# Kernel optimization log

Measured on AMD Instinct MI355X. Metric: run time of the kernel, lower is better.

The kernel has to match this reference:

```python
import jax, jax.numpy as jnp
import numpy as np

N_EMBED = 1024
N_HEAD = 16
B, T = 4, 2048
EPS = 1e-5


def setup_inputs() -> dict:
    key = jax.random.key(0)
    ks = jax.random.split(key, 8)
    s = 0.02
    return {
        "x": jax.random.normal(ks[0], (B, T, N_EMBED), dtype=jnp.float32),
        "ln1_w": jnp.ones((N_EMBED,), jnp.float32),
        "ln1_b": jnp.zeros((N_EMBED,), jnp.float32),
        "w_qkv": jax.random.normal(ks[1], (N_EMBED, 3 * N_EMBED), dtype=jnp.float32) * s,
        "b_qkv": jnp.zeros((3 * N_EMBED,), jnp.float32),
        "w_o": jax.random.normal(ks[2], (N_EMBED, N_EMBED), dtype=jnp.float32) * s,
        "b_o": jnp.zeros((N_EMBED,), jnp.float32),
        "ln2_w": jnp.ones((N_EMBED,), jnp.float32),
        "ln2_b": jnp.zeros((N_EMBED,), jnp.float32),
        "w_fc": jax.random.normal(ks[3], (N_EMBED, 4 * N_EMBED), dtype=jnp.float32) * s,
        "b_fc": jnp.zeros((4 * N_EMBED,), jnp.float32),
        "w_proj": jax.random.normal(ks[4], (4 * N_EMBED, N_EMBED), dtype=jnp.float32) * s,
        "b_proj": jnp.zeros((N_EMBED,), jnp.float32),
    }


def _layernorm(x, w, b):
    mu = jnp.mean(x, axis=-1, keepdims=True)
    var = jnp.mean(jnp.square(x - mu), axis=-1, keepdims=True)
    return (x - mu) * jax.lax.rsqrt(var + EPS) * w + b


def _attention(x, w_qkv, b_qkv, w_o, b_o):
    b, t, c = x.shape
    hd = c // N_HEAD
    qkv = x @ w_qkv + b_qkv                      # [B,T,3C]
    q, k, v = jnp.split(qkv, 3, axis=-1)
    # [B,H,T,hd]
    q = q.reshape(b, t, N_HEAD, hd).transpose(0, 2, 1, 3)
    k = k.reshape(b, t, N_HEAD, hd).transpose(0, 2, 1, 3)
    v = v.reshape(b, t, N_HEAD, hd).transpose(0, 2, 1, 3)
    scale = 1.0 / np.sqrt(hd).astype(np.float32)
    scores = jnp.einsum('bhqd,bhkd->bhqk', q, k) * scale  # [B,H,T,T]
    mask = jnp.tril(jnp.ones((t, t), dtype=bool))
    scores = jnp.where(mask, scores, -jnp.inf)
    attn = jax.nn.softmax(scores, axis=-1)
    ctx = jnp.einsum('bhqk,bhkd->bhqd', attn, v)  # [B,H,T,hd]
    ctx = ctx.transpose(0, 2, 1, 3).reshape(b, t, c)
    return ctx @ w_o + b_o


def reference(x, ln1_w, ln1_b, w_qkv, b_qkv, w_o, b_o,
              ln2_w, ln2_b, w_fc, b_fc, w_proj, b_proj):
    # x = x + attn(ln1(x))
    x = x + _attention(_layernorm(x, ln1_w, ln1_b), w_qkv, b_qkv, w_o, b_o)
    # x = x + mlp(ln2(x))
    h = _layernorm(x, ln2_w, ln2_b)
    h = jax.nn.gelu(h @ w_fc + b_fc, approximate=False)
    x = x + (h @ w_proj + b_proj)
    return x
```

## Files before the change

kernel.cpp:

```cpp
#include <hip/hip_runtime.h>
#include <hip/hip_bf16.h>
#include <math.h>

#define N_EMBED 1024
#define N_HEAD 16
#define HD 64
#define BB 4
#define TT 2048
#define NTOK (BB * TT)
#define QKV_LD (3 * N_EMBED)

typedef __bf16 bf16x8 __attribute__((ext_vector_type(8)));
typedef float f32x4 __attribute__((ext_vector_type(4)));

__device__ __forceinline__ unsigned short f2bf(float f) {
    __hip_bfloat16 h = __float2bfloat16(f);
    return __builtin_bit_cast(unsigned short, h);
}

__device__ __forceinline__ void gll16(const unsigned short* g, unsigned short* l) {
    __builtin_amdgcn_global_load_lds(
        (const __attribute__((address_space(1))) void*)g,
        (__attribute__((address_space(3))) void*)l,
        16, 0, 0);
}

__global__ __launch_bounds__(256) void transpose_bf16_kernel(
    const float* __restrict__ in, unsigned short* __restrict__ out, int K, int N) {
    __shared__ float tile[32][33];
    int bx = blockIdx.x * 32;
    int by = blockIdx.y * 32;
    int tx = threadIdx.x, ty = threadIdx.y;
#pragma unroll
    for (int i = ty; i < 32; i += 8)
        tile[i][tx] = in[(size_t)(by + i) * N + bx + tx];
    __syncthreads();
#pragma unroll
    for (int i = ty; i < 32; i += 8)
        out[(size_t)(bx + i) * K + by + tx] = f2bf(tile[tx][i]);
}

__global__ __launch_bounds__(256) void transpose_v_kernel(
    const unsigned short* __restrict__ qkv, unsigned short* __restrict__ vt) {
    __shared__ unsigned short tile[32][33];
    int z = blockIdx.z;
    int b = z >> 4, h = z & 15;
    int t0 = blockIdx.x * 32, d0 = blockIdx.y * 32;
    int tx = threadIdx.x, ty = threadIdx.y;
    const unsigned short* src = qkv + (size_t)(b * TT) * QKV_LD + 2 * N_EMBED + h * HD;
#pragma unroll
    for (int i = ty; i < 32; i += 8)
        tile[i][tx] = src[(size_t)(t0 + i) * QKV_LD + d0 + tx];
    __syncthreads();
    unsigned short* dst = vt + (size_t)z * HD * TT;
#pragma unroll
    for (int i = ty; i < 32; i += 8)
        dst[(size_t)(d0 + i) * TT + t0 + tx] = tile[tx][i];
}

__global__ __launch_bounds__(256) void ln_kernel(
    const float* __restrict__ x, const float* __restrict__ w,
    const float* __restrict__ b, unsigned short* __restrict__ out) {
    int row = blockIdx.x;
    int t = threadIdx.x;
    const float* xr = x + (size_t)row * N_EMBED;
    float4 v = reinterpret_cast<const float4*>(xr)[t];
    float s = v.x + v.y + v.z + v.w;
    float s2 = v.x * v.x + v.y * v.y + v.z * v.z + v.w * v.w;
#pragma unroll
    for (int m = 1; m < 64; m <<= 1) {
        s += __shfl_xor(s, m);
        s2 += __shfl_xor(s2, m);
    }
    __shared__ float red[8];
    int wv = t >> 6, ln = t & 63;
    if (ln == 0) { red[wv] = s; red[wv + 4] = s2; }
    __syncthreads();
    s = red[0] + red[1] + red[2] + red[3];
    s2 = red[4] + red[5] + red[6] + red[7];
    float mu = s * (1.0f / N_EMBED);
    float var = s2 * (1.0f / N_EMBED) - mu * mu;
    float r = rsqrtf(var + 1e-5f);
    float4 wv4 = reinterpret_cast<const float4*>(w)[t];
    float4 bv4 = reinterpret_cast<const float4*>(b)[t];
    ushort4 o;
    o.x = f2bf((v.x - mu) * r * wv4.x + bv4.x);
    o.y = f2bf((v.y - mu) * r * wv4.y + bv4.y);
    o.z = f2bf((v.z - mu) * r * wv4.z + bv4.z);
    o.w = f2bf((v.w - mu) * r * wv4.w + bv4.w);
    *reinterpret_cast<ushort4*>(out + (size_t)row * N_EMBED + t * 4) = o;
}

template <int EPI>
__global__ __launch_bounds__(256) void gemm_kernel(
    const unsigned short* __restrict__ A,
    const unsigned short* __restrict__ BT,
    const float* __restrict__ bias,
    const float* __restrict__ resid,
    float* __restrict__ outf,
    unsigned short* __restrict__ outb,
    int M, int N, int K) {
    __shared__ __align__(16) unsigned short As[128 * 32];
    __shared__ __align__(16) unsigned short Bs[128 * 32];
    int nbn = N >> 7;
    int nwg = gridDim.x;
    int orig = blockIdx.x;
    int swz = (orig & 7) * (nwg >> 3) + (orig >> 3);
    int bm = swz / nbn, bn = swz % nbn;
    int t = threadIdx.x;
    int lane = t & 63, wv = t >> 6;
    int wm = wv >> 1, wn = wv & 1;
    int mr = lane & 15, kg = lane >> 4;

    f32x4 acc[4][4];
#pragma unroll
    for (int i = 0; i < 4; i++)
#pragma unroll
        for (int j = 0; j < 4; j++) acc[i][j] = (f32x4){0.f, 0.f, 0.f, 0.f};

    int srow = t >> 2, sq = t & 3;
    const unsigned short* gA1 = A + (size_t)(bm * 128 + srow) * K + sq * 8;
    const unsigned short* gA2 = gA1 + (size_t)64 * K;
    const unsigned short* gB1 = BT + (size_t)(bn * 128 + srow) * K + sq * 8;
    const unsigned short* gB2 = gB1 + (size_t)64 * K;
    int w512 = (t >> 6) * 512;

    for (int k0 = 0; k0 < K; k0 += 32) {
        __syncthreads();
        gll16(gA1 + k0, As + w512);
        gll16(gA2 + k0, As + 2048 + w512);
        gll16(gB1 + k0, Bs + w512);
        gll16(gB2 + k0, Bs + 2048 + w512);
        __syncthreads();
        bf16x8 af[4], bfr[4];
#pragma unroll
        for (int i = 0; i < 4; i++)
            af[i] = *reinterpret_cast<const bf16x8*>(&As[(wm * 64 + i * 16 + mr) * 32 + kg * 8]);
#pragma unroll
        for (int j = 0; j < 4; j++)
            bfr[j] = *reinterpret_cast<const bf16x8*>(&Bs[(wn * 64 + j * 16 + mr) * 32 + kg * 8]);
#pragma unroll
        for (int i = 0; i < 4; i++)
#pragma unroll
            for (int j = 0; j < 4; j++)
                acc[i][j] = __builtin_amdgcn_mfma_f32_16x16x32_bf16(af[i], bfr[j], acc[i][j], 0, 0, 0);
    }

#pragma unroll
    for (int i = 0; i < 4; i++)
#pragma unroll
        for (int j = 0; j < 4; j++) {
            int n = bn * 128 + wn * 64 + j * 16 + mr;
            float bs = bias[n];
#pragma unroll
            for (int r = 0; r < 4; r++) {
                int m = bm * 128 + wm * 64 + i * 16 + kg * 4 + r;
                size_t idx = (size_t)m * N + n;
                float v = acc[i][j][r] + bs;
                if (EPI == 0) {
                    outb[idx] = f2bf(v);
                } else if (EPI == 1) {
                    outf[idx] = v + resid[idx];
                } else {
                    float g = 0.5f * v * (1.0f + erff(v * 0.70710678118f));
                    outb[idx] = f2bf(g);
                }
            }
        }
}

__global__ __launch_bounds__(256, 4) void attn_kernel(
    const unsigned short* __restrict__ qkv,
    const unsigned short* __restrict__ vt,
    unsigned short* __restrict__ ctx) {
    __shared__ __align__(16) unsigned short Kb[2][4096];
    __shared__ __align__(16) unsigned short Vb[2][4096];
    __shared__ __align__(16) unsigned short PL[4096];
    int t = threadIdx.x, lane = t & 63, wv = t >> 6;
    int mr = lane & 15, kg = lane >> 4;
    const float SCL = 0.18033688011112042f;

    int srow[2], scol[2], sbase[2];
#pragma unroll
    for (int i = 0; i < 2; i++) {
        int L = i * 256 + wv * 64 + lane;
        int row = L >> 3, slot = L & 7;
        srow[i] = row;
        scol[i] = (slot ^ (row & 7)) * 8;
        sbase[i] = (i * 256 + wv * 64) * 8;
    }
    const int csw = mr & 7;

#pragma unroll
    for (int item = 0; item < 2; ++item) {
        int wid = (item == 0) ? (int)blockIdx.x : (2047 - (int)blockIdx.x);
        int qt = wid >> 6;
        int bh = wid & 63;
        int h = bh & 15, b = bh >> 4;
        int qbase = qt * 64 + wv * 16;

        const unsigned short* qp = qkv + (size_t)(b * TT) * QKV_LD + h * HD;
        const unsigned short* kp = qp + N_EMBED;
        const unsigned short* vtp = vt + (size_t)bh * HD * TT;

        bf16x8 aq[2];
#pragma unroll
        for (int c = 0; c < 2; c++)
            aq[c] = *reinterpret_cast<const bf16x8*>(
                qp + (size_t)(qbase + mr) * QKV_LD + c * 32 + kg * 8);

        f32x4 Oa[4];
#pragma unroll
        for (int jd = 0; jd < 4; jd++) Oa[jd] = (f32x4){0.f, 0.f, 0.f, 0.f};
        float mrow[4] = {-3.0e38f, -3.0e38f, -3.0e38f, -3.0e38f};
        float lrow[4] = {0.f, 0.f, 0.f, 0.f};

#pragma unroll
        for (int i = 0; i < 2; i++) {
            gll16(kp + (size_t)srow[i] * QKV_LD + scol[i], &Kb[0][sbase[i]]);
            gll16(vtp + (size_t)srow[i] * TT + scol[i], &Vb[0][sbase[i]]);
        }
        __syncthreads();

        for (int tile = 0; tile <= qt; ++tile) {
            int cur = tile & 1;
            int kv0 = tile * 64;
            if (tile < qt) {
                int nkv = kv0 + 64;
#pragma unroll
                for (int i = 0; i < 2; i++) {
                    gll16(kp + (size_t)(nkv + srow[i]) * QKV_LD + scol[i], &Kb[cur ^ 1][sbase[i]]);
                    gll16(vtp + (size_t)srow[i] * TT + nkv + scol[i], &Vb[cur ^ 1][sbase[i]]);
                }
            }

            f32x4 sf[4];
#pragma unroll
            for (int j = 0; j < 4; j++) {
                int rl = j * 16 + mr;
                f32x4 s = (f32x4){0.f, 0.f, 0.f, 0.f};
#pragma unroll
                for (int c = 0; c < 2; c++) {
                    bf16x8 bk = *reinterpret_cast<const bf16x8*>(
                        &Kb[cur][rl * 64 + ((4 * c + kg) ^ csw) * 8]);
                    s = __builtin_amdgcn_mfma_f32_16x16x32_bf16(aq[c], bk, s, 0, 0, 0);
                }
                sf[j] = s;
            }

            float tmax[4];
            if (tile == qt) {
#pragma unroll
                for (int r = 0; r < 4; r++) {
                    int qrow = qbase + kg * 4 + r;
                    float mx = -3.0e38f;
#pragma unroll
                    for (int j = 0; j < 4; j++) {
                        int kc = kv0 + j * 16 + mr;
                        float sv = sf[j][r] * SCL;
                        if (kc > qrow) sv = -3.0e38f;
                        sf[j][r] = sv;
                        mx = fmaxf(mx, sv);
                    }
                    tmax[r] = mx;
                }
            } else {
#pragma unroll
                for (int r = 0; r < 4; r++) {
                    float mx = -3.0e38f;
#pragma unroll
                    for (int j = 0; j < 4; j++) {
                        float sv = sf[j][r] * SCL;
                        sf[j][r] = sv;
                        mx = fmaxf(mx, sv);
                    }
                    tmax[r] = mx;
                }
            }
#pragma unroll
            for (int r = 0; r < 4; r++) {
#pragma unroll
                for (int m = 1; m < 16; m <<= 1) tmax[r] = fmaxf(tmax[r], __shfl_xor(tmax[r], m));
            }
#pragma unroll
            for (int r = 0; r < 4; r++) {
                float mn = fmaxf(mrow[r], tmax[r]);
                float alpha = __builtin_amdgcn_exp2f(mrow[r] - mn);
                mrow[r] = mn;
                lrow[r] *= alpha;
#pragma unroll
                for (int jd = 0; jd < 4; jd++) Oa[jd][r] *= alpha;
            }
            float rsum[4] = {0.f, 0.f, 0.f, 0.f};
#pragma unroll
            for (int j = 0; j < 4; j++)
#pragma unroll
                for (int r = 0; r < 4; r++) {
                    float p = __builtin_amdgcn_exp2f(sf[j][r] - mrow[r]);
                    sf[j][r] = p;
                    rsum[r] += p;
                }
#pragma unroll
            for (int r = 0; r < 4; r++) {
#pragma unroll
                for (int m = 1; m < 16; m <<= 1) rsum[r] += __shfl_xor(rsum[r], m);
                lrow[r] += rsum[r];
            }

#pragma unroll
            for (int r = 0; r < 4; r++) {
                int qrow = wv * 16 + kg * 4 + r;
                int base = qrow * 64;
                int sw = (qrow & 7) << 3;
#pragma unroll
                for (int j = 0; j < 4; j++)
                    PL[(base + j * 16 + mr) ^ sw] = f2bf(sf[j][r]);
            }

#pragma unroll
            for (int c = 0; c < 2; c++) {
                bf16x8 pa = *reinterpret_cast<const bf16x8*>(
                    &PL[(wv * 16 + mr) * 64 + ((4 * c + kg) ^ csw) * 8]);
#pragma unroll
                for (int jd = 0; jd < 4; jd++) {
                    int rv = jd * 16 + mr;
                    bf16x8 vb = *reinterpret_cast<const bf16x8*>(
                        &Vb[cur][rv * 64 + ((4 * c + kg) ^ csw) * 8]);
                    Oa[jd] = __builtin_amdgcn_mfma_f32_16x16x32_bf16(pa, vb, Oa[jd], 0, 0, 0);
                }
            }
            __syncthreads();
        }

        float inv[4];
#pragma unroll
        for (int r = 0; r < 4; r++) inv[r] = 1.0f / lrow[r];
#pragma unroll
        for (int jd = 0; jd < 4; jd++)
#pragma unroll
            for (int r = 0; r < 4; r++) {
                int q = qbase + kg * 4 + r;
                ctx[(size_t)(b * TT + q) * N_EMBED + h * HD + jd * 16 + mr] =
                    f2bf(Oa[jd][r] * inv[r]);
            }
    }
}

extern "C" void kernel_launch(void* const* d_in, const int* in_sizes, int n_in,
                              void* d_out, int out_size, void* d_ws, size_t ws_size,
                              hipStream_t stream) {
    const float* x      = (const float*)d_in[0];
    const float* ln1_w  = (const float*)d_in[1];
    const float* ln1_b  = (const float*)d_in[2];
    const float* w_qkv  = (const float*)d_in[3];
    const float* b_qkv  = (const float*)d_in[4];
    const float* w_o    = (const float*)d_in[5];
    const float* b_o    = (const float*)d_in[6];
    const float* ln2_w  = (const float*)d_in[7];
    const float* ln2_b  = (const float*)d_in[8];
    const float* w_fc   = (const float*)d_in[9];
    const float* b_fc   = (const float*)d_in[10];
    const float* w_proj = (const float*)d_in[11];
    const float* b_proj = (const float*)d_in[12];
    float* out = (float*)d_out;

    char* ws = (char*)d_ws;
    size_t off = 0;
    auto alloc = [&](size_t bytes) -> void* {
        void* p = ws + off;
        off += (bytes + 255) & ~(size_t)255;
        return p;
    };
    unsigned short* wqkv_t  = (unsigned short*)alloc((size_t)3072 * 1024 * 2);
    unsigned short* wo_t    = (unsigned short*)alloc((size_t)1024 * 1024 * 2);
    unsigned short* wfc_t   = (unsigned short*)alloc((size_t)4096 * 1024 * 2);
    unsigned short* wproj_t = (unsigned short*)alloc((size_t)1024 * 4096 * 2);
    unsigned short* lnb     = (unsigned short*)alloc((size_t)NTOK * 1024 * 2);
    float*          x1      = (float*)alloc((size_t)NTOK * 1024 * 4);
    unsigned short* qkv     = (unsigned short*)alloc((size_t)NTOK * 3072 * 2);
    unsigned short* ctxb    = (unsigned short*)alloc((size_t)NTOK * 1024 * 2);
    unsigned short* hbuf    = qkv;
    unsigned short* vt      = (unsigned short*)x1;

    dim3 tb32(32, 8);
    transpose_bf16_kernel<<<dim3(3072 / 32, 1024 / 32), tb32, 0, stream>>>(w_qkv, wqkv_t, 1024, 3072);
    transpose_bf16_kernel<<<dim3(1024 / 32, 1024 / 32), tb32, 0, stream>>>(w_o, wo_t, 1024, 1024);
    transpose_bf16_kernel<<<dim3(4096 / 32, 1024 / 32), tb32, 0, stream>>>(w_fc, wfc_t, 1024, 4096);
    transpose_bf16_kernel<<<dim3(1024 / 32, 4096 / 32), tb32, 0, stream>>>(w_proj, wproj_t, 4096, 1024);

    ln_kernel<<<NTOK, 256, 0, stream>>>(x, ln1_w, ln1_b, lnb);
    gemm_kernel<0><<<(NTOK / 128) * (3072 / 128), 256, 0, stream>>>(
        lnb, wqkv_t, b_qkv, nullptr, nullptr, qkv, NTOK, 3072, 1024);
    transpose_v_kernel<<<dim3(TT / 32, HD / 32, BB * N_HEAD), tb32, 0, stream>>>(qkv, vt);
    attn_kernel<<<1024, 256, 0, stream>>>(qkv, vt, ctxb);
    gemm_kernel<1><<<(NTOK / 128) * (1024 / 128), 256, 0, stream>>>(
        ctxb, wo_t, b_o, x, x1, nullptr, NTOK, 1024, 1024);
    ln_kernel<<<NTOK, 256, 0, stream>>>(x1, ln2_w, ln2_b, lnb);
    gemm_kernel<2><<<(NTOK / 128) * (4096 / 128), 256, 0, stream>>>(
        lnb, wfc_t, b_fc, nullptr, nullptr, hbuf, NTOK, 4096, 1024);
    gemm_kernel<1><<<(NTOK / 128) * (1024 / 128), 256, 0, stream>>>(
        hbuf, wproj_t, b_proj, x1, out, nullptr, NTOK, 1024, 4096);
}
```

Baseline: 469.4 us.

## Pack K/V into contiguous tiles and load attention fragments directly into registers

Replaces the V transpose kernel with a pack kernel that writes K and transposed V into contiguous 64x64 tiles per head. The attention kernel then drops its LDS K/V double buffers and global_load_lds, and instead loads MFMA fragments straight from global memory into registers, double-buffering K and removing the per-tile block barrier. It also launches one block per query tile (2048 blocks, in bh-major order) instead of pairing light and heavy tiles per block, and drops the occupancy hint. The aim is to cut LDS traffic and synchronisation, at the cost of more register pressure, uncoalesced-looking per-lane global reads that rely on cache reuse across the four waves, and causal load imbalance across blocks.

```diff
diff --git a/kernel.cpp b/kernel.cpp
--- a/kernel.cpp
+++ b/kernel.cpp
@@ -40,22 +40,39 @@
         out[(size_t)(bx + i) * K + by + tx] = f2bf(tile[tx][i]);
 }
 
-__global__ __launch_bounds__(256) void transpose_v_kernel(
-    const unsigned short* __restrict__ qkv, unsigned short* __restrict__ vt) {
-    __shared__ unsigned short tile[32][33];
-    int z = blockIdx.z;
-    int b = z >> 4, h = z & 15;
-    int t0 = blockIdx.x * 32, d0 = blockIdx.y * 32;
-    int tx = threadIdx.x, ty = threadIdx.y;
-    const unsigned short* src = qkv + (size_t)(b * TT) * QKV_LD + 2 * N_EMBED + h * HD;
-#pragma unroll
-    for (int i = ty; i < 32; i += 8)
-        tile[i][tx] = src[(size_t)(t0 + i) * QKV_LD + d0 + tx];
+__global__ __launch_bounds__(256) void pack_kv_kernel(
+    const unsigned short* __restrict__ qkv,
+    unsigned short* __restrict__ kpk, unsigned short* __restrict__ vpk) {
+    __shared__ unsigned short vt_[64][65];
+    int blk = blockIdx.x;
+    int bh = blk >> 5, tile = blk & 31;
+    int b = bh >> 4, h = bh & 15;
+    int t = threadIdx.x;
+    int kv = t >> 2, dq = (t & 3) * 16;
+    const unsigned short* base =
+        qkv + (size_t)(b * TT + tile * 64 + kv) * QKV_LD + h * HD + dq;
+
+    uint4 k0 = *reinterpret_cast<const uint4*>(base + N_EMBED);
+    uint4 k1 = *reinterpret_cast<const uint4*>(base + N_EMBED + 8);
+    unsigned short* kdst = kpk + (size_t)blk * 4096 + kv * 64 + dq;
+    *reinterpret_cast<uint4*>(kdst) = k0;
+    *reinterpret_cast<uint4*>(kdst + 8) = k1;
+
+    uint4 v0 = *reinterpret_cast<const uint4*>(base + 2 * N_EMBED);
+    uint4 v1 = *reinterpret_cast<const uint4*>(base + 2 * N_EMBED + 8);
+    unsigned short tmp[16];
+    *reinterpret_cast<uint4*>(tmp) = v0;
+    *reinterpret_cast<uint4*>(tmp + 8) = v1;
+#pragma unroll
+    for (int e = 0; e < 16; e++) vt_[kv][dq + e] = tmp[e];
     __syncthreads();
-    unsigned short* dst = vt + (size_t)z * HD * TT;
-#pragma unroll
-    for (int i = ty; i < 32; i += 8)
-        dst[(size_t)(d0 + i) * TT + t0 + tx] = tile[tx][i];
+    int dd = t >> 2, kq = (t & 3) * 16;
+    unsigned short o[16];
+#pragma unroll
+    for (int e = 0; e < 16; e++) o[e] = vt_[kq + e][dd];
+    unsigned short* vdst = vpk + (size_t)blk * 4096 + dd * 64 + kq;
+    *reinterpret_cast<uint4*>(vdst) = *reinterpret_cast<uint4*>(o);
+    *reinterpret_cast<uint4*>(vdst + 8) = *reinterpret_cast<uint4*>(o + 8);
 }
 
 __global__ __launch_bounds__(256) void ln_kernel(
@@ -169,181 +186,169 @@
         }
 }
 
-__global__ __launch_bounds__(256, 4) void attn_kernel(
+__global__ __launch_bounds__(256) void attn_kernel(
     const unsigned short* __restrict__ qkv,
-    const unsigned short* __restrict__ vt,
+    const unsigned short* __restrict__ kpk,
+    const unsigned short* __restrict__ vpk,
     unsigned short* __restrict__ ctx) {
-    __shared__ __align__(16) unsigned short Kb[2][4096];
-    __shared__ __align__(16) unsigned short Vb[2][4096];
     __shared__ __align__(16) unsigned short PL[4096];
     int t = threadIdx.x, lane = t & 63, wv = t >> 6;
     int mr = lane & 15, kg = lane >> 4;
     const float SCL = 0.18033688011112042f;
 
-    int srow[2], scol[2], sbase[2];
-#pragma unroll
-    for (int i = 0; i < 2; i++) {
-        int L = i * 256 + wv * 64 + lane;
-        int row = L >> 3, slot = L & 7;
-        srow[i] = row;
-        scol[i] = (slot ^ (row & 7)) * 8;
-        sbase[i] = (i * 256 + wv * 64) * 8;
+    int wid = blockIdx.x;
+    int bh = wid >> 5, qt = wid & 31;
+    int h = bh & 15, b = bh >> 4;
+    int qbase = qt * 64 + wv * 16;
+
+    const unsigned short* qp = qkv + (size_t)(b * TT) * QKV_LD + h * HD;
+    const unsigned short* kb = kpk + (size_t)bh * 32 * 4096;
+    const unsigned short* vb = vpk + (size_t)bh * 32 * 4096;
+
+    bf16x8 aq[2];
+#pragma unroll
+    for (int c = 0; c < 2; c++)
+        aq[c] = *reinterpret_cast<const bf16x8*>(
+            qp + (size_t)(qbase + mr) * QKV_LD + c * 32 + kg * 8);
+
+    f32x4 Oa[4];
+#pragma unroll
+    for (int jd = 0; jd < 4; jd++) Oa[jd] = (f32x4){0.f, 0.f, 0.f, 0.f};
+    float mrow[4] = {-3.0e38f, -3.0e38f, -3.0e38f, -3.0e38f};
+    float lrow[4] = {0.f, 0.f, 0.f, 0.f};
+
+    auto loadK = [&](bf16x8 (&Kf)[4][2], int tile) {
+        const unsigned short* kt = kb + (size_t)tile * 4096;
+#pragma unroll
+        for (int j = 0; j < 4; j++)
+#pragma unroll
+            for (int c = 0; c < 2; c++)
+                Kf[j][c] = *reinterpret_cast<const bf16x8*>(
+                    kt + (j * 16 + mr) * 64 + c * 32 + kg * 8);
+    };
+
+    auto compute = [&](bf16x8 (&Kf)[4][2], int tile) {
+        int kv0 = tile * 64;
+        f32x4 sf[4];
+#pragma unroll
+        for (int j = 0; j < 4; j++) {
+            f32x4 s = (f32x4){0.f, 0.f, 0.f, 0.f};
+#pragma unroll
+            for (int c = 0; c < 2; c++)
+                s = __builtin_amdgcn_mfma_f32_16x16x32_bf16(aq[c], Kf[j][c], s, 0, 0, 0);
+            sf[j] = s;
+        }
+        bf16x8 vf[4][2];
+        const unsigned short* vtile = vb + (size_t)tile * 4096;
+#pragma unroll
+        for (int jd = 0; jd < 4; jd++)
+#pragma unroll
+            for (int c = 0; c < 2; c++)
+                vf[jd][c] = *reinterpret_cast<const bf16x8*>(
+                    vtile + (jd * 16 + mr) * 64 + c * 32 + kg * 8);
+
+        float tmax[4];
+        if (tile == qt) {
+#pragma unroll
+            for (int r = 0; r < 4; r++) {
+                int qrow = qbase + kg * 4 + r;
+                float mx = -3.0e38f;
+#pragma unroll
+                for (int j = 0; j < 4; j++) {
+                    int kc = kv0 + j * 16 + mr;
+                    float sv = sf[j][r] * SCL;
+                    if (kc > qrow) sv = -3.0e38f;
+                    sf[j][r] = sv;
+                    mx = fmaxf(mx, sv);
+                }
+                tmax[r] = mx;
+            }
+        } else {
+#pragma unroll
+            for (int r = 0; r < 4; r++) {
+                float mx = -3.0e38f;
+#pragma unroll
+                for (int j = 0; j < 4; j++) {
+                    float sv = sf[j][r] * SCL;
+                    sf[j][r] = sv;
+                    mx = fmaxf(mx, sv);
+                }
+                tmax[r] = mx;
+            }
+        }
+#pragma unroll
+        for (int r = 0; r < 4; r++) {
+#pragma unroll
+            for (int m = 1; m < 16; m <<= 1) tmax[r] = fmaxf(tmax[r], __shfl_xor(tmax[r], m));
+        }
+#pragma unroll
+        for (int r = 0; r < 4; r++) {
+            float mn = fmaxf(mrow[r], tmax[r]);
+            float alpha = __builtin_amdgcn_exp2f(mrow[r] - mn);
+            mrow[r] = mn;
+            lrow[r] *= alpha;
+#pragma unroll
+            for (int jd = 0; jd < 4; jd++) Oa[jd][r] *= alpha;
+        }
+        float rsum[4] = {0.f, 0.f, 0.f, 0.f};
+#pragma unroll
+        for (int j = 0; j < 4; j++)
+#pragma unroll
+            for (int r = 0; r < 4; r++) {
+                float p = __builtin_amdgcn_exp2f(sf[j][r] - mrow[r]);
+                sf[j][r] = p;
+                rsum[r] += p;
+            }
+#pragma unroll
+        for (int r = 0; r < 4; r++) {
+#pragma unroll
+            for (int m = 1; m < 16; m <<= 1) rsum[r] += __shfl_xor(rsum[r], m);
+            lrow[r] += rsum[r];
+        }
+
+#pragma unroll
+        for (int r = 0; r < 4; r++) {
+            int qrow = wv * 16 + kg * 4 + r;
+            int base = qrow * 64;
+            int sw = (qrow & 7) << 3;
+#pragma unroll
+            for (int j = 0; j < 4; j++)
+                PL[(base + j * 16 + mr) ^ sw] = f2bf(sf[j][r]);
+        }
+        const int csw = mr & 7;
+#pragma unroll
+        for (int c = 0; c < 2; c++) {
+            bf16x8 pa = *reinterpret_cast<const bf16x8*>(
+                &PL[(wv * 16 + mr) * 64 + ((4 * c + kg) ^ csw) * 8]);
+#pragma unroll
+            for (int jd = 0; jd < 4; jd++)
+                Oa[jd] = __builtin_amdgcn_mfma_f32_16x16x32_bf16(pa, vf[jd][c], Oa[jd], 0, 0, 0);
+        }
+    };
+
+    bf16x8 K0[4][2], K1[4][2];
+    loadK(K0, 0);
+    int tile = 0;
+    while (true) {
+        if (tile + 1 <= qt) loadK(K1, tile + 1);
+        compute(K0, tile);
+        if (++tile > qt) break;
+        if (tile + 1 <= qt) loadK(K0, tile + 1);
+        compute(K1, tile);
+        if (++tile > qt) break;
     }
-    const int csw = mr & 7;
-
-#pragma unroll
-    for (int item = 0; item < 2; ++item) {
-        int wid = (item == 0) ? (int)blockIdx.x : (2047 - (int)blockIdx.x);
-        int qt = wid >> 6;
-        int bh = wid & 63;
-        int h = bh & 15, b = bh >> 4;
-        int qbase = qt * 64 + wv * 16;
-
-        const unsigned short* qp = qkv + (size_t)(b * TT) * QKV_LD + h * HD;
-        const unsigned short* kp = qp + N_EMBED;
-        const unsigned short* vtp = vt + (size_t)bh * HD * TT;
-
-        bf16x8 aq[2];
-#pragma unroll
-        for (int c = 0; c < 2; c++)
-            aq[c] = *reinterpret_cast<const bf16x8*>(
-                qp + (size_t)(qbase + mr) * QKV_LD + c * 32 + kg * 8);
-
-        f32x4 Oa[4];
-#pragma unroll
-        for (int jd = 0; jd < 4; jd++) Oa[jd] = (f32x4){0.f, 0.f, 0.f, 0.f};
-        float mrow[4] = {-3.0e38f, -3.0e38f, -3.0e38f, -3.0e38f};
-        float lrow[4] = {0.f, 0.f, 0.f, 0.f};
-
-#pragma unroll
-        for (int i = 0; i < 2; i++) {
-            gll16(kp + (size_t)srow[i] * QKV_LD + scol[i], &Kb[0][sbase[i]]);
-            gll16(vtp + (size_t)srow[i] * TT + scol[i], &Vb[0][sbase[i]]);
-        }
-        __syncthreads();
-
-        for (int tile = 0; tile <= qt; ++tile) {
-            int cur = tile & 1;
-            int kv0 = tile * 64;
-            if (tile < qt) {
-                int nkv = kv0 + 64;
-#pragma unroll
-                for (int i = 0; i < 2; i++) {
-                    gll16(kp + (size_t)(nkv + srow[i]) * QKV_LD + scol[i], &Kb[cur ^ 1][sbase[i]]);
-                    gll16(vtp + (size_t)srow[i] * TT + nkv + scol[i], &Vb[cur ^ 1][sbase[i]]);
-                }
-            }
-
-            f32x4 sf[4];
-#pragma unroll
-            for (int j = 0; j < 4; j++) {
-                int rl = j * 16 + mr;
-                f32x4 s = (f32x4){0.f, 0.f, 0.f, 0.f};
-#pragma unroll
-                for (int c = 0; c < 2; c++) {
-                    bf16x8 bk = *reinterpret_cast<const bf16x8*>(
-                        &Kb[cur][rl * 64 + ((4 * c + kg) ^ csw) * 8]);
-                    s = __builtin_amdgcn_mfma_f32_16x16x32_bf16(aq[c], bk, s, 0, 0, 0);
-                }
-                sf[j] = s;
-            }
-
-            float tmax[4];
-            if (tile == qt) {
-#pragma unroll
-                for (int r = 0; r < 4; r++) {
-                    int qrow = qbase + kg * 4 + r;
-                    float mx = -3.0e38f;
-#pragma unroll
-                    for (int j = 0; j < 4; j++) {
-                        int kc = kv0 + j * 16 + mr;
-                        float sv = sf[j][r] * SCL;
-                        if (kc > qrow) sv = -3.0e38f;
-                        sf[j][r] = sv;
-                        mx = fmaxf(mx, sv);
-                    }
-                    tmax[r] = mx;
-                }
-            } else {
-#pragma unroll
-                for (int r = 0; r < 4; r++) {
-                    float mx = -3.0e38f;
-#pragma unroll
-                    for (int j = 0; j < 4; j++) {
-                        float sv = sf[j][r] * SCL;
-                        sf[j][r] = sv;
-                        mx = fmaxf(mx, sv);
-                    }
-                    tmax[r] = mx;
-                }
-            }
-#pragma unroll
-            for (int r = 0; r < 4; r++) {
-#pragma unroll
-                for (int m = 1; m < 16; m <<= 1) tmax[r] = fmaxf(tmax[r], __shfl_xor(tmax[r], m));
-            }
-#pragma unroll
-            for (int r = 0; r < 4; r++) {
-                float mn = fmaxf(mrow[r], tmax[r]);
-                float alpha = __builtin_amdgcn_exp2f(mrow[r] - mn);
-                mrow[r] = mn;
-                lrow[r] *= alpha;
-#pragma unroll
-                for (int jd = 0; jd < 4; jd++) Oa[jd][r] *= alpha;
-            }
-            float rsum[4] = {0.f, 0.f, 0.f, 0.f};
-#pragma unroll
-            for (int j = 0; j < 4; j++)
-#pragma unroll
-                for (int r = 0; r < 4; r++) {
-                    float p = __builtin_amdgcn_exp2f(sf[j][r] - mrow[r]);
-                    sf[j][r] = p;
-                    rsum[r] += p;
-                }
-#pragma unroll
-            for (int r = 0; r < 4; r++) {
-#pragma unroll
-                for (int m = 1; m < 16; m <<= 1) rsum[r] += __shfl_xor(rsum[r], m);
-                lrow[r] += rsum[r];
-            }
-
-#pragma unroll
-            for (int r = 0; r < 4; r++) {
-                int qrow = wv * 16 + kg * 4 + r;
-                int base = qrow * 64;
-                int sw = (qrow & 7) << 3;
-#pragma unroll
-                for (int j = 0; j < 4; j++)
-                    PL[(base + j * 16 + mr) ^ sw] = f2bf(sf[j][r]);
-            }
-
-#pragma unroll
-            for (int c = 0; c < 2; c++) {
-                bf16x8 pa = *reinterpret_cast<const bf16x8*>(
-                    &PL[(wv * 16 + mr) * 64 + ((4 * c + kg) ^ csw) * 8]);
-#pragma unroll
-                for (int jd = 0; jd < 4; jd++) {
-                    int rv = jd * 16 + mr;
-                    bf16x8 vb = *reinterpret_cast<const bf16x8*>(
-                        &Vb[cur][rv * 64 + ((4 * c + kg) ^ csw) * 8]);
-                    Oa[jd] = __builtin_amdgcn_mfma_f32_16x16x32_bf16(pa, vb, Oa[jd], 0, 0, 0);
-                }
-            }
-            __syncthreads();
-        }
-
-        float inv[4];
-#pragma unroll
-        for (int r = 0; r < 4; r++) inv[r] = 1.0f / lrow[r];
-#pragma unroll
-        for (int jd = 0; jd < 4; jd++)
-#pragma unroll
-            for (int r = 0; r < 4; r++) {
-                int q = qbase + kg * 4 + r;
-                ctx[(size_t)(b * TT + q) * N_EMBED + h * HD + jd * 16 + mr] =
-                    f2bf(Oa[jd][r] * inv[r]);
-            }
-    }
+
+    float inv[4];
+#pragma unroll
+    for (int r = 0; r < 4; r++) inv[r] = 1.0f / lrow[r];
+#pragma unroll
+    for (int jd = 0; jd < 4; jd++)
+#pragma unroll
+        for (int r = 0; r < 4; r++) {
+            int q = qbase + kg * 4 + r;
+            ctx[(size_t)(b * TT + q) * N_EMBED + h * HD + jd * 16 + mr] =
+                f2bf(Oa[jd][r] * inv[r]);
+        }
 }
 
 extern "C" void kernel_launch(void* const* d_in, const int* in_sizes, int n_in,
@@ -380,7 +385,8 @@
     unsigned short* qkv     = (unsigned short*)alloc((size_t)NTOK * 3072 * 2);
     unsigned short* ctxb    = (unsigned short*)alloc((size_t)NTOK * 1024 * 2);
     unsigned short* hbuf    = qkv;
-    unsigned short* vt      = (unsigned short*)x1;
+    unsigned short* kpk     = (unsigned short*)x1;
+    unsigned short* vpk     = kpk + (size_t)64 * 32 * 4096;
 
     dim3 tb32(32, 8);
     transpose_bf16_kernel<<<dim3(3072 / 32, 1024 / 32), tb32, 0, stream>>>(w_qkv, wqkv_t, 1024, 3072);
@@ -391,8 +397,8 @@
     ln_kernel<<<NTOK, 256, 0, stream>>>(x, ln1_w, ln1_b, lnb);
     gemm_kernel<0><<<(NTOK / 128) * (3072 / 128), 256, 0, stream>>>(
         lnb, wqkv_t, b_qkv, nullptr, nullptr, qkv, NTOK, 3072, 1024);
-    transpose_v_kernel<<<dim3(TT / 32, HD / 32, BB * N_HEAD), tb32, 0, stream>>>(qkv, vt);
-    attn_kernel<<<1024, 256, 0, stream>>>(qkv, vt, ctxb);
+    pack_kv_kernel<<<64 * 32, 256, 0, stream>>>(qkv, kpk, vpk);
+    attn_kernel<<<2048, 256, 0, stream>>>(qkv, kpk, vpk, ctxb);
     gemm_kernel<1><<<(NTOK / 128) * (1024 / 128), 256, 0, stream>>>(
         ctxb, wo_t, b_o, x, x1, nullptr, NTOK, 1024, 1024);
     ln_kernel<<<NTOK, 256, 0, stream>>>(x1, ln2_w, ln2_b, lnb);
```

Result: slower. 805.4 us (+71.6%).

## Enlarge attention query tile to 128 and triple-buffer K/V loads

Applied to the files above, without the earlier changes.

The attention kernel now processes 128 query rows per block, with each wave handling two 16-row fragments. Each K/V fragment read from LDS is reused across both fragments, which halves the K/V staging traffic per query. K/V tiles are triple-buffered with explicit vmcnt waits and a single barrier per tile, prefetching two tiles ahead. The grid is halved to 512 blocks, each pairing a light and a heavy causal tile for balance. In exchange, register and LDS use rise, the launch-bounds occupancy hint is dropped, and fewer blocks are available to fill the GPU.

```diff
diff --git a/kernel.cpp b/kernel.cpp
--- a/kernel.cpp
+++ b/kernel.cpp
@@ -169,16 +169,24 @@
         }
 }
 
-__global__ __launch_bounds__(256, 4) void attn_kernel(
+__global__ __launch_bounds__(256) void attn_kernel(
     const unsigned short* __restrict__ qkv,
     const unsigned short* __restrict__ vt,
     unsigned short* __restrict__ ctx) {
-    __shared__ __align__(16) unsigned short Kb[2][4096];
-    __shared__ __align__(16) unsigned short Vb[2][4096];
-    __shared__ __align__(16) unsigned short PL[4096];
+    __shared__ __align__(16) unsigned short Kb[3][4096];
+    __shared__ __align__(16) unsigned short Vb[3][4096];
+    __shared__ __align__(16) unsigned short PL[8192];
+    const float SCL = 0.18033688011112042f;
     int t = threadIdx.x, lane = t & 63, wv = t >> 6;
     int mr = lane & 15, kg = lane >> 4;
-    const float SCL = 0.18033688011112042f;
+
+    int wid = blockIdx.x;
+    int bh = wid >> 3, qp2 = wid & 7;
+    int h = bh & 15, b = bh >> 4;
+
+    const unsigned short* qptr = qkv + (size_t)(b * TT) * QKV_LD + h * HD;
+    const unsigned short* kp = qptr + N_EMBED;
+    const unsigned short* vtp = vt + (size_t)bh * HD * TT;
 
     int srow[2], scol[2], sbase[2];
 #pragma unroll
@@ -191,158 +199,157 @@
     }
     const int csw = mr & 7;
 
-#pragma unroll
+    auto stage = [&](int tile, int bi) {
+        int kv0 = tile * 64;
+#pragma unroll
+        for (int i = 0; i < 2; i++) {
+            gll16(kp + (size_t)(kv0 + srow[i]) * QKV_LD + scol[i], &Kb[bi][sbase[i]]);
+            gll16(vtp + (size_t)srow[i] * TT + kv0 + scol[i], &Vb[bi][sbase[i]]);
+        }
+    };
+
     for (int item = 0; item < 2; ++item) {
-        int wid = (item == 0) ? (int)blockIdx.x : (2047 - (int)blockIdx.x);
-        int qt = wid >> 6;
-        int bh = wid & 63;
-        int h = bh & 15, b = bh >> 4;
-        int qbase = qt * 64 + wv * 16;
-
-        const unsigned short* qp = qkv + (size_t)(b * TT) * QKV_LD + h * HD;
-        const unsigned short* kp = qp + N_EMBED;
-        const unsigned short* vtp = vt + (size_t)bh * HD * TT;
-
-        bf16x8 aq[2];
-#pragma unroll
-        for (int c = 0; c < 2; c++)
-            aq[c] = *reinterpret_cast<const bf16x8*>(
-                qp + (size_t)(qbase + mr) * QKV_LD + c * 32 + kg * 8);
-
-        f32x4 Oa[4];
-#pragma unroll
-        for (int jd = 0; jd < 4; jd++) Oa[jd] = (f32x4){0.f, 0.f, 0.f, 0.f};
-        float mrow[4] = {-3.0e38f, -3.0e38f, -3.0e38f, -3.0e38f};
-        float lrow[4] = {0.f, 0.f, 0.f, 0.f};
-
-#pragma unroll
-        for (int i = 0; i < 2; i++) {
-            gll16(kp + (size_t)srow[i] * QKV_LD + scol[i], &Kb[0][sbase[i]]);
-            gll16(vtp + (size_t)srow[i] * TT + scol[i], &Vb[0][sbase[i]]);
-        }
-        __syncthreads();
-
-        for (int tile = 0; tile <= qt; ++tile) {
-            int cur = tile & 1;
-            int kv0 = tile * 64;
-            if (tile < qt) {
-                int nkv = kv0 + 64;
-#pragma unroll
-                for (int i = 0; i < 2; i++) {
-                    gll16(kp + (size_t)(nkv + srow[i]) * QKV_LD + scol[i], &Kb[cur ^ 1][sbase[i]]);
-                    gll16(vtp + (size_t)srow[i] * TT + nkv + scol[i], &Vb[cur ^ 1][sbase[i]]);
-                }
+        int qt = (item == 0) ? qp2 : 15 - qp2;
+        int ntiles = 2 * qt + 2;
+        int qbase = qt * 128 + wv * 32;
+
+        bf16x8 aq[2][2];
+#pragma unroll
+        for (int f = 0; f < 2; f++)
+#pragma unroll
+            for (int c = 0; c < 2; c++)
+                aq[f][c] = *reinterpret_cast<const bf16x8*>(
+                    qptr + (size_t)(qbase + f * 16 + mr) * QKV_LD + c * 32 + kg * 8);
+
+        f32x4 Oa[2][4];
+#pragma unroll
+        for (int f = 0; f < 2; f++)
+#pragma unroll
+            for (int jd = 0; jd < 4; jd++) Oa[f][jd] = (f32x4){0.f, 0.f, 0.f, 0.f};
+        float mrow[2][4], lrow[2][4];
+#pragma unroll
+        for (int f = 0; f < 2; f++)
+#pragma unroll
+            for (int r = 0; r < 4; r++) { mrow[f][r] = -3.0e38f; lrow[f][r] = 0.f; }
+
+        stage(0, 0);
+        stage(1, 1);
+
+        for (int tl = 0; tl < ntiles; ++tl) {
+            if (tl + 1 < ntiles) {
+                asm volatile("s_waitcnt vmcnt(4)" ::: "memory");
+            } else {
+                asm volatile("s_waitcnt vmcnt(0)" ::: "memory");
             }
-
-            f32x4 sf[4];
+            __builtin_amdgcn_s_barrier();
+            int t2 = tl + 2;
+            if (t2 < ntiles) stage(t2, t2 % 3);
+
+            int bi = tl % 3;
+            int kv0 = tl * 64;
+            const unsigned short* Kt = Kb[bi];
+            const unsigned short* Vt = Vb[bi];
+
+            f32x4 sf[2][4];
 #pragma unroll
             for (int j = 0; j < 4; j++) {
                 int rl = j * 16 + mr;
-                f32x4 s = (f32x4){0.f, 0.f, 0.f, 0.f};
-#pragma unroll
-                for (int c = 0; c < 2; c++) {
-                    bf16x8 bk = *reinterpret_cast<const bf16x8*>(
-                        &Kb[cur][rl * 64 + ((4 * c + kg) ^ csw) * 8]);
-                    s = __builtin_amdgcn_mfma_f32_16x16x32_bf16(aq[c], bk, s, 0, 0, 0);
-                }
-                sf[j] = s;
+                bf16x8 bk0 = *reinterpret_cast<const bf16x8*>(&Kt[rl * 64 + (kg ^ csw) * 8]);
+                bf16x8 bk1 = *reinterpret_cast<const bf16x8*>(&Kt[rl * 64 + ((4 + kg) ^ csw) * 8]);
+#pragma unroll
+                for (int f = 0; f < 2; f++) {
+                    f32x4 s = (f32x4){0.f, 0.f, 0.f, 0.f};
+                    s = __builtin_amdgcn_mfma_f32_16x16x32_bf16(aq[f][0], bk0, s, 0, 0, 0);
+                    s = __builtin_amdgcn_mfma_f32_16x16x32_bf16(aq[f][1], bk1, s, 0, 0, 0);
+                    sf[f][j] = s;
+                }
             }
 
-            float tmax[4];
-            if (tile == qt) {
+            bool dmask = (tl >= 2 * qt);
+#pragma unroll
+            for (int f = 0; f < 2; f++) {
+                float tmax[4];
 #pragma unroll
                 for (int r = 0; r < 4; r++) {
-                    int qrow = qbase + kg * 4 + r;
+                    int qrow = qbase + f * 16 + kg * 4 + r;
                     float mx = -3.0e38f;
 #pragma unroll
                     for (int j = 0; j < 4; j++) {
-                        int kc = kv0 + j * 16 + mr;
-                        float sv = sf[j][r] * SCL;
-                        if (kc > qrow) sv = -3.0e38f;
-                        sf[j][r] = sv;
+                        float sv = sf[f][j][r] * SCL;
+                        if (dmask && (kv0 + j * 16 + mr > qrow)) sv = -3.0e38f;
+                        sf[f][j][r] = sv;
                         mx = fmaxf(mx, sv);
                     }
                     tmax[r] = mx;
                 }
-            } else {
 #pragma unroll
                 for (int r = 0; r < 4; r++) {
-                    float mx = -3.0e38f;
-#pragma unroll
-                    for (int j = 0; j < 4; j++) {
-                        float sv = sf[j][r] * SCL;
-                        sf[j][r] = sv;
-                        mx = fmaxf(mx, sv);
+#pragma unroll
+                    for (int m = 1; m < 16; m <<= 1)
+                        tmax[r] = fmaxf(tmax[r], __shfl_xor(tmax[r], m));
+                    float mn = fmaxf(mrow[f][r], tmax[r]);
+                    float al = __builtin_amdgcn_exp2f(mrow[f][r] - mn);
+                    mrow[f][r] = mn;
+                    lrow[f][r] *= al;
+#pragma unroll
+                    for (int jd = 0; jd < 4; jd++) Oa[f][jd][r] *= al;
+                }
+                float rsum[4] = {0.f, 0.f, 0.f, 0.f};
+#pragma unroll
+                for (int j = 0; j < 4; j++)
+#pragma unroll
+                    for (int r = 0; r < 4; r++) {
+                        float p = __builtin_amdgcn_exp2f(sf[f][j][r] - mrow[f][r]);
+                        sf[f][j][r] = p;
+                        rsum[r] += p;
                     }
-                    tmax[r] = mx;
+#pragma unroll
+                for (int r = 0; r < 4; r++) {
+#pragma unroll
+                    for (int m = 1; m < 16; m <<= 1) rsum[r] += __shfl_xor(rsum[r], m);
+                    lrow[f][r] += rsum[r];
+                }
+#pragma unroll
+                for (int r = 0; r < 4; r++) {
+                    int rowL = wv * 32 + f * 16 + kg * 4 + r;
+                    int base = rowL * 64;
+                    int sw = (rowL & 7) << 3;
+#pragma unroll
+                    for (int j = 0; j < 4; j++)
+                        PL[(base + j * 16 + mr) ^ sw] = f2bf(sf[f][j][r]);
                 }
             }
-#pragma unroll
-            for (int r = 0; r < 4; r++) {
-#pragma unroll
-                for (int m = 1; m < 16; m <<= 1) tmax[r] = fmaxf(tmax[r], __shfl_xor(tmax[r], m));
+
+#pragma unroll
+            for (int c = 0; c < 2; c++) {
+                int ch = ((4 * c + kg) ^ csw) * 8;
+                bf16x8 pa0 = *reinterpret_cast<const bf16x8*>(&PL[(wv * 32 + mr) * 64 + ch]);
+                bf16x8 pa1 = *reinterpret_cast<const bf16x8*>(&PL[(wv * 32 + 16 + mr) * 64 + ch]);
+#pragma unroll
+                for (int jd = 0; jd < 4; jd++) {
+                    bf16x8 vf = *reinterpret_cast<const bf16x8*>(&Vt[(jd * 16 + mr) * 64 + ch]);
+                    Oa[0][jd] = __builtin_amdgcn_mfma_f32_16x16x32_bf16(pa0, vf, Oa[0][jd], 0, 0, 0);
+                    Oa[1][jd] = __builtin_amdgcn_mfma_f32_16x16x32_bf16(pa1, vf, Oa[1][jd], 0, 0, 0);
+                }
             }
-#pragma unroll
-            for (int r = 0; r < 4; r++) {
-                float mn = fmaxf(mrow[r], tmax[r]);
-                float alpha = __builtin_amdgcn_exp2f(mrow[r] - mn);
-                mrow[r] = mn;
-                lrow[r] *= alpha;
-#pragma unroll
-                for (int jd = 0; jd < 4; jd++) Oa[jd][r] *= alpha;
-            }
-            float rsum[4] = {0.f, 0.f, 0.f, 0.f};
-#pragma unroll
-            for (int j = 0; j < 4; j++)
+        }
+
+        float inv[2][4];
+#pragma unroll
+        for (int f = 0; f < 2; f++)
+#pragma unroll
+            for (int r = 0; r < 4; r++) inv[f][r] = 1.0f / lrow[f][r];
+#pragma unroll
+        for (int f = 0; f < 2; f++)
+#pragma unroll
+            for (int jd = 0; jd < 4; jd++)
 #pragma unroll
                 for (int r = 0; r < 4; r++) {
-                    float p = __builtin_amdgcn_exp2f(sf[j][r] - mrow[r]);
-                    sf[j][r] = p;
-                    rsum[r] += p;
-                }
-#pragma unroll
-            for (int r = 0; r < 4; r++) {
-#pragma unroll
-                for (int m = 1; m < 16; m <<= 1) rsum[r] += __shfl_xor(rsum[r], m);
-                lrow[r] += rsum[r];
-            }
-
-#pragma unroll
-            for (int r = 0; r < 4; r++) {
-                int qrow = wv * 16 + kg * 4 + r;
-                int base = qrow * 64;
-                int sw = (qrow & 7) << 3;
-#pragma unroll
-                for (int j = 0; j < 4; j++)
-                    PL[(base + j * 16 + mr) ^ sw] = f2bf(sf[j][r]);
-            }
-
-#pragma unroll
-            for (int c = 0; c < 2; c++) {
-                bf16x8 pa = *reinterpret_cast<const bf16x8*>(
-                    &PL[(wv * 16 + mr) * 64 + ((4 * c + kg) ^ csw) * 8]);
-#pragma unroll
-                for (int jd = 0; jd < 4; jd++) {
-                    int rv = jd * 16 + mr;
-                    bf16x8 vb = *reinterpret_cast<const bf16x8*>(
-                        &Vb[cur][rv * 64 + ((4 * c + kg) ^ csw) * 8]);
-                    Oa[jd] = __builtin_amdgcn_mfma_f32_16x16x32_bf16(pa, vb, Oa[jd], 0, 0, 0);
-                }
-            }
-            __syncthreads();
-        }
-
-        float inv[4];
-#pragma unroll
-        for (int r = 0; r < 4; r++) inv[r] = 1.0f / lrow[r];
-#pragma unroll
-        for (int jd = 0; jd < 4; jd++)
-#pragma unroll
-            for (int r = 0; r < 4; r++) {
-                int q = qbase + kg * 4 + r;
-                ctx[(size_t)(b * TT + q) * N_EMBED + h * HD + jd * 16 + mr] =
-                    f2bf(Oa[jd][r] * inv[r]);
-            }
+                    int q = qbase + f * 16 + kg * 4 + r;
+                    ctx[(size_t)(b * TT + q) * N_EMBED + h * HD + jd * 16 + mr] =
+                        f2bf(Oa[f][jd][r] * inv[f][r]);
+                }
+        __syncthreads();
     }
 }
 
@@ -392,7 +399,7 @@
     gemm_kernel<0><<<(NTOK / 128) * (3072 / 128), 256, 0, stream>>>(
         lnb, wqkv_t, b_qkv, nullptr, nullptr, qkv, NTOK, 3072, 1024);
     transpose_v_kernel<<<dim3(TT / 32, HD / 32, BB * N_HEAD), tb32, 0, stream>>>(qkv, vt);
-    attn_kernel<<<1024, 256, 0, stream>>>(qkv, vt, ctxb);
+    attn_kernel<<<512, 256, 0, stream>>>(qkv, vt, ctxb);
     gemm_kernel<1><<<(NTOK / 128) * (1024 / 128), 256, 0, stream>>>(
         ctxb, wo_t, b_o, x, x1, nullptr, NTOK, 1024, 1024);
     ln_kernel<<<NTOK, 256, 0, stream>>>(x1, ln2_w, ln2_b, lnb);
```

Result: slower. 550.6 us (+17.3%).
